# Optimization experiments

Hardware: AMD Instinct MI355X
Metric: run time of the kernel (lower is better)

## Reference

```python
import jax, jax.numpy as jnp
import numpy as np

EPS = 1e-5

def _bn(x, g, b):
    # training-mode BatchNorm1d: batch statistics (biased variance), eps=1e-5
    mean = jnp.mean(x, axis=0)
    var = jnp.mean(jnp.square(x - mean), axis=0)
    return (x - mean) * jax.lax.rsqrt(var + EPS) * g + b

def setup_inputs() -> dict:
    key = jax.random.key(0)
    ks = jax.random.split(key, 16)
    n_nodes, n_edges, d_h, d_e = 50000, 800000, 128, 64
    in_feats, h1, h2, out_feats = 2 * d_h + d_e, 256, 128, 1
    def lin(k, fi, fo):
        bound = 1.0 / np.sqrt(fi)
        kw, kb = jax.random.split(k)
        W = jax.random.uniform(kw, (fo, fi), jnp.float32, -bound, bound)
        b = jax.random.uniform(kb, (fo,), jnp.float32, -bound, bound)
        return W, b
    W1, b1 = lin(ks[0], in_feats, h1)
    W2, b2 = lin(ks[1], h1, h2)
    W3, b3 = lin(ks[2], h2, out_feats)
    return {
        "h": jax.random.normal(ks[3], (n_nodes, d_h), jnp.float32),
        "e": jax.random.normal(ks[4], (n_edges, d_e), jnp.float32),
        "src": jax.random.randint(ks[5], (n_edges,), 0, n_nodes, jnp.int32),
        "dst": jax.random.randint(ks[6], (n_edges,), 0, n_nodes, jnp.int32),
        "bn0_g": jnp.ones((in_feats,), jnp.float32), "bn0_b": jnp.zeros((in_feats,), jnp.float32),
        "W1": W1, "b1": b1,
        "bn1_g": jnp.ones((h1,), jnp.float32), "bn1_b": jnp.zeros((h1,), jnp.float32),
        "W2": W2, "b2": b2,
        "bn2_g": jnp.ones((h2,), jnp.float32), "bn2_b": jnp.zeros((h2,), jnp.float32),
        "W3": W3, "b3": b3,
    }

def reference(h, e, src, dst, bn0_g, bn0_b, W1, b1, bn1_g, bn1_b, W2, b2, bn2_g, bn2_b, W3, b3):
    # edge gather + concat: [n_edges, 2*d_h + d_e]
    x = jnp.concatenate([h[src], h[dst], e], axis=1)
    x = _bn(x, bn0_g, bn0_b)
    x = jnp.maximum(x @ W1.T + b1, 0.0)  # Linear + ReLU (dropout = identity, deterministic)
    x = _bn(x, bn1_g, bn1_b)
    x = jnp.maximum(x @ W2.T + b2, 0.0)
    x = _bn(x, bn2_g, bn2_b)
    return x @ W3.T + b3
```

## Files before the change

kernel.cpp:

```cpp
#include <hip/hip_runtime.h>


#define N_EDGES 800000
#define N_NODES 50000

typedef __attribute__((ext_vector_type(8))) short bf8_t;
typedef __attribute__((ext_vector_type(4))) float f4_t;
typedef __attribute__((ext_vector_type(2))) unsigned int u2_t;
typedef __attribute__((ext_vector_type(4))) unsigned int u4_t;

__device__ __forceinline__ unsigned short f2bf(float f) {
    unsigned int u = __builtin_bit_cast(unsigned int, f);
    u += 0x7FFFu + ((u >> 16) & 1u);
    return (unsigned short)(u >> 16);
}
__device__ __forceinline__ float bf2f(unsigned short s) {
    unsigned int u = ((unsigned int)s) << 16;
    return __builtin_bit_cast(float, u);
}
__device__ __forceinline__ bf8_t cvt8(f4_t x, f4_t y) {
    bf8_t r;
    r[0] = (short)f2bf(x[0]); r[1] = (short)f2bf(x[1]);
    r[2] = (short)f2bf(x[2]); r[3] = (short)f2bf(x[3]);
    r[4] = (short)f2bf(y[0]); r[5] = (short)f2bf(y[1]);
    r[6] = (short)f2bf(y[2]); r[7] = (short)f2bf(y[3]);
    return r;
}

__global__ __launch_bounds__(256) void k_hist(const int* __restrict__ src, const int* __restrict__ dst,
                                              int* __restrict__ cs, int* __restrict__ cd) {
    int i = blockIdx.x * 256 + threadIdx.x;
    if (i < N_EDGES) {
        atomicAdd(&cs[src[i]], 1);
        atomicAdd(&cd[dst[i]], 1);
    }
}

__global__ __launch_bounds__(256) void k_ecvt(const float* __restrict__ e,
        unsigned short* __restrict__ ebf, float* __restrict__ sum, float* __restrict__ sq) {
    const int tid = threadIdx.x;
    const int lane = tid & 63;
    const int cg = tid & 7, rr = tid >> 3;
    f4_t sa = {0.f,0.f,0.f,0.f}, sb = sa, qa = sa, qb = sa;
    for (int r = blockIdx.x * 32 + rr; r < N_EDGES; r += gridDim.x * 32) {
        f4_t va = __builtin_nontemporal_load((const f4_t*)(e + (size_t)r * 64 + cg * 8));
        f4_t vb = __builtin_nontemporal_load((const f4_t*)(e + (size_t)r * 64 + cg * 8 + 4));
        sa += va; qa += va * va; sb += vb; qb += vb * vb;
        bf8_t o = cvt8(va, vb);
        __builtin_nontemporal_store(o,
            (bf8_t*)(ebf + (size_t)(r >> 4) * 1024 + (cg >> 2) * 512 + (((r & 15) << 2) + (cg & 3)) * 8));
    }
#pragma unroll
    for (int d = 8; d <= 32; d <<= 1) {
#pragma unroll
        for (int j = 0; j < 4; ++j) {
            sa[j] += __shfl_xor(sa[j], d); qa[j] += __shfl_xor(qa[j], d);
            sb[j] += __shfl_xor(sb[j], d); qb[j] += __shfl_xor(qb[j], d);
        }
    }
    __shared__ float red[128];
    if (tid < 128) red[tid] = 0.f;
    __syncthreads();
    if (lane < 8) {
#pragma unroll
        for (int j = 0; j < 4; ++j) {
            atomicAdd(&red[lane * 8 + j], sa[j]);
            atomicAdd(&red[lane * 8 + 4 + j], sb[j]);
            atomicAdd(&red[64 + lane * 8 + j], qa[j]);
            atomicAdd(&red[64 + lane * 8 + 4 + j], qb[j]);
        }
    }
    __syncthreads();
    if (tid < 64) atomicAdd(&sum[256 + tid], red[tid]);
    else if (tid < 128) atomicAdd(&sq[256 + tid - 64], red[tid]);
}

__global__ __launch_bounds__(256) void k_hstats(const float* __restrict__ h,
                                                const int* __restrict__ cs, const int* __restrict__ cd,
                                                float* __restrict__ sum, float* __restrict__ sq) {
    const int tid = threadIdx.x;
    const int c = tid & 127, g = tid >> 7;
    float ss = 0.f, qs = 0.f, sd = 0.f, qd = 0.f;
    for (int n = blockIdx.x * 2 + g; n < N_NODES; n += gridDim.x * 2) {
        float v = h[(size_t)n * 128 + c];
        float a = (float)cs[n], b = (float)cd[n];
        ss += a * v; qs += a * v * v;
        sd += b * v; qd += b * v * v;
    }
    __shared__ float red[256];
    red[tid] = ss; __syncthreads();
    if (tid < 128) atomicAdd(&sum[tid], red[tid] + red[tid + 128]);
    __syncthreads();
    red[tid] = qs; __syncthreads();
    if (tid < 128) atomicAdd(&sq[tid], red[tid] + red[tid + 128]);
    __syncthreads();
    red[tid] = sd; __syncthreads();
    if (tid < 128) atomicAdd(&sum[128 + tid], red[tid] + red[tid + 128]);
    __syncthreads();
    red[tid] = qd; __syncthreads();
    if (tid < 128) atomicAdd(&sq[128 + tid], red[tid] + red[tid + 128]);
}

__global__ __launch_bounds__(320) void k_fold0(const float* __restrict__ sum, const float* __restrict__ sq,
        const float* __restrict__ g0, const float* __restrict__ b0,
        float* __restrict__ scale0, float* __restrict__ shift0) {
    int j = threadIdx.x;
    if (j < 320) {
        const float invE = 1.f / (float)N_EDGES;
        float mu = sum[j] * invE;
        float var = sq[j] * invE - mu * mu;
        float sc = g0[j] * rsqrtf(var + 1e-5f);
        scale0[j] = sc;
        shift0[j] = b0[j] - mu * sc;
    }
}

__global__ __launch_bounds__(320) void k_foldW1(const float* __restrict__ W1, const float* __restrict__ b1,
        const float* __restrict__ scale0, const float* __restrict__ shift0,
        unsigned short* __restrict__ W1s, unsigned short* __restrict__ W1d,
        unsigned short* __restrict__ W1e, float* __restrict__ b1p) {
    __shared__ float sc[320], sh[320];
    const int tid = threadIdx.x;
    if (tid < 320) { sc[tid] = scale0[tid]; sh[tid] = shift0[tid]; }
    __syncthreads();
    if (tid < 256) {
        float acc = b1[tid];
        const float* wr = W1 + (size_t)tid * 320;
        for (int j = 0; j < 320; ++j) {
            float wv = wr[j];
            acc += wv * sh[j];
            unsigned short wb = f2bf(wv * sc[j]);
            if (j < 128) W1s[tid * 128 + j] = wb;
            else if (j < 256) W1d[tid * 128 + (j - 128)] = wb;
            else W1e[tid * 64 + (j - 256)] = wb;
        }
        b1p[tid] = acc;
    }
}

__global__ __launch_bounds__(256) void k_P(const float* __restrict__ h,
        const unsigned short* __restrict__ W1s, const unsigned short* __restrict__ W1d,
        unsigned short* __restrict__ Ps, unsigned short* __restrict__ Pd) {
    __shared__ unsigned short tile[16 * 264];
    const int tid = threadIdx.x;
    const int w = tid >> 6, lane = tid & 63, quad = lane >> 4, l15 = lane & 15;
    const unsigned short* W = blockIdx.y ? W1d : W1s;
    unsigned short* P = blockIdx.y ? Pd : Ps;
    const size_t base = (size_t)blockIdx.x * 256;
    bf8_t bfr[4][4];
#pragma unroll
    for (int j = 0; j < 4; ++j) {
        const unsigned short* wp = W + (size_t)((w * 4 + j) * 16 + l15) * 128 + quad * 8;
#pragma unroll
        for (int ks = 0; ks < 4; ++ks) bfr[j][ks] = *(const bf8_t*)(wp + ks * 32);
    }
    const int erow = tid >> 4, ex = tid & 15;
    for (int mc = 0; mc < 16; ++mc) {
        const size_t row0 = base + mc * 16;
        size_t ar = row0 + l15; if (ar >= N_NODES) ar = N_NODES - 1;
        const float* hp = h + ar * 128 + quad * 8;
        bf8_t af[4];
#pragma unroll
        for (int ks = 0; ks < 4; ++ks)
            af[ks] = cvt8(*(const f4_t*)(hp + ks * 32), *(const f4_t*)(hp + ks * 32 + 4));
#pragma unroll
        for (int j = 0; j < 4; ++j) {
            f4_t t = {0.f, 0.f, 0.f, 0.f};
#pragma unroll
            for (int ks = 0; ks < 4; ++ks)
                t = __builtin_amdgcn_mfma_f32_16x16x32_bf16(af[ks], bfr[j][ks], t, 0, 0, 0);
#pragma unroll
            for (int r = 0; r < 4; ++r)
                tile[(quad * 4 + r) * 264 + (w * 4 + j) * 16 + l15] = f2bf(t[r]);
        }
        __syncthreads();
        const size_t orow = row0 + erow;
        if (orow < N_NODES) {
            u4_t v0 = *(const u4_t*)(tile + erow * 264 + ex * 16);
            u4_t v1 = *(const u4_t*)(tile + erow * 264 + ex * 16 + 8);
            *(u4_t*)(P + orow * 256 + ex * 16) = v0;
            *(u4_t*)(P + orow * 256 + ex * 16 + 8) = v1;
        }
        __syncthreads();
    }
}

__global__ __launch_bounds__(256) void k_stats1(const unsigned short* __restrict__ ebf,
        const int* __restrict__ src, const int* __restrict__ dst,
        const unsigned short* __restrict__ Ps, const unsigned short* __restrict__ Pd,
        const unsigned short* __restrict__ W1e, const float* __restrict__ b1p,
        float* __restrict__ slots) {
    __shared__ int sIdx[256], dIdx[256];
    const int tid = threadIdx.x;
    const int w = tid >> 6, lane = tid & 63, quad = lane >> 4, l15 = lane & 15;
    const int perm = l15 * 4 + quad;
    const size_t base = (size_t)blockIdx.x * 256;
    const size_t blk16 = (size_t)blockIdx.x * 16;
    sIdx[tid] = src[base + tid];
    dIdx[tid] = dst[base + tid];
    bf8_t bfr[4][2];
    float bias4[4];
#pragma unroll
    for (int j = 0; j < 4; ++j) {
        const unsigned short* wp = W1e + (size_t)((w * 4 + j) * 16 + l15) * 64 + quad * 8;
        bfr[j][0] = *(const bf8_t*)(wp);
        bfr[j][1] = *(const bf8_t*)(wp + 32);
        bias4[j] = b1p[(w * 4 + j) * 16 + l15];
    }
    const int cb = w * 64 + l15;
    float s[4] = {0.f, 0.f, 0.f, 0.f}, q[4] = {0.f, 0.f, 0.f, 0.f};
    __syncthreads();
    bf8_t af0, af1;
    {
        const unsigned short* ap = ebf + blk16 * 1024 + perm * 8;
        af0 = __builtin_nontemporal_load((const bf8_t*)(ap));
        af1 = __builtin_nontemporal_load((const bf8_t*)(ap + 512));
    }
    for (int mc = 0; mc < 16; ++mc) {
        const int r0 = mc * 16 + quad * 4;
        const unsigned short* p0 = Ps + (size_t)sIdx[r0 + 0] * 256 + cb;
        const unsigned short* p1 = Ps + (size_t)sIdx[r0 + 1] * 256 + cb;
        const unsigned short* p2 = Ps + (size_t)sIdx[r0 + 2] * 256 + cb;
        const unsigned short* p3 = Ps + (size_t)sIdx[r0 + 3] * 256 + cb;
        const unsigned short* d0 = Pd + (size_t)dIdx[r0 + 0] * 256 + cb;
        const unsigned short* d1 = Pd + (size_t)dIdx[r0 + 1] * 256 + cb;
        const unsigned short* d2 = Pd + (size_t)dIdx[r0 + 2] * 256 + cb;
        const unsigned short* d3 = Pd + (size_t)dIdx[r0 + 3] * 256 + cb;
        unsigned short ps[4][4], pd[4][4];
#pragma unroll
        for (int j = 0; j < 4; ++j) {
            ps[0][j] = p0[j * 16]; ps[1][j] = p1[j * 16];
            ps[2][j] = p2[j * 16]; ps[3][j] = p3[j * 16];
            pd[0][j] = d0[j * 16]; pd[1][j] = d1[j * 16];
            pd[2][j] = d2[j * 16]; pd[3][j] = d3[j * 16];
        }
        f4_t acc[4];
#pragma unroll
        for (int j = 0; j < 4; ++j) {
            f4_t t = {0.f, 0.f, 0.f, 0.f};
            t = __builtin_amdgcn_mfma_f32_16x16x32_bf16(af0, bfr[j][0], t, 0, 0, 0);
            acc[j] = __builtin_amdgcn_mfma_f32_16x16x32_bf16(af1, bfr[j][1], t, 0, 0, 0);
        }
        if (mc < 15) {
            const unsigned short* ap = ebf + (blk16 + mc + 1) * 1024 + perm * 8;
            af0 = __builtin_nontemporal_load((const bf8_t*)(ap));
            af1 = __builtin_nontemporal_load((const bf8_t*)(ap + 512));
        }
#pragma unroll
        for (int j = 0; j < 4; ++j)
#pragma unroll
            for (int r = 0; r < 4; ++r) {
                float v = acc[j][r] + bf2f(ps[r][j]) + bf2f(pd[r][j]) + bias4[j];
                v = fmaxf(v, 0.f);
                s[j] += v; q[j] += v * v;
            }
    }
#pragma unroll
    for (int j = 0; j < 4; ++j) {
        s[j] += __shfl_xor(s[j], 16); s[j] += __shfl_xor(s[j], 32);
        q[j] += __shfl_xor(q[j], 16); q[j] += __shfl_xor(q[j], 32);
    }
    if (lane < 16) {
        float* sl = slots + (size_t)(blockIdx.x & 63) * 512;
#pragma unroll
        for (int j = 0; j < 4; ++j) {
            atomicAdd(&sl[cb + j * 16], s[j]);
            atomicAdd(&sl[256 + cb + j * 16], q[j]);
        }
    }
}

__global__ __launch_bounds__(256) void k_fold1(const float* __restrict__ slots,
        const float* __restrict__ g1, const float* __restrict__ b1n,
        const float* __restrict__ W2, const float* __restrict__ b2,
        unsigned short* __restrict__ W2p, float* __restrict__ b2p) {
    __shared__ float sc[256], sh[256];
    const int tid = threadIdx.x;
    float S = 0.f, Q = 0.f;
    for (int s = 0; s < 64; ++s) { S += slots[s * 512 + tid]; Q += slots[s * 512 + 256 + tid]; }
    const float invE = 1.f / (float)N_EDGES;
    float mu = S * invE;
    float var = Q * invE - mu * mu;
    float scl = g1[tid] * rsqrtf(var + 1e-5f);
    sc[tid] = scl; sh[tid] = b1n[tid] - mu * scl;
    __syncthreads();
    if (tid < 128) {
        float acc = b2[tid];
        const float* wr = W2 + (size_t)tid * 256;
        for (int j = 0; j < 256; ++j) {
            float wv = wr[j];
            acc += wv * sh[j];
            W2p[tid * 256 + j] = f2bf(wv * sc[j]);
        }
        b2p[tid] = acc;
    }
}

__global__ __launch_bounds__(256) void k_L12(const unsigned short* __restrict__ ebf,
        const int* __restrict__ src, const int* __restrict__ dst,
        const unsigned short* __restrict__ Ps, const unsigned short* __restrict__ Pd,
        const unsigned short* __restrict__ W1e, const float* __restrict__ b1p,
        const unsigned short* __restrict__ W2p, const float* __restrict__ b2p,
        unsigned short* __restrict__ a2c, float* __restrict__ slots) {
    __shared__ unsigned short tile1[16 * 264];
    __shared__ unsigned short tile2[2][4096];
    __shared__ int sIdx[256], dIdx[256];
    const int tid = threadIdx.x;
    const int w = tid >> 6, lane = tid & 63, quad = lane >> 4, l15 = lane & 15;
    const int perm = l15 * 4 + quad;
    const size_t base = (size_t)blockIdx.x * 256;
    const size_t blk16 = (size_t)blockIdx.x * 16;
    sIdx[tid] = src[base + tid];
    dIdx[tid] = dst[base + tid];
    bf8_t bfr1[4][2];
    float bias4[4];
#pragma unroll
    for (int j = 0; j < 4; ++j) {
        const unsigned short* wp = W1e + (size_t)((w * 4 + j) * 16 + l15) * 64 + quad * 8;
        bfr1[j][0] = *(const bf8_t*)(wp);
        bfr1[j][1] = *(const bf8_t*)(wp + 32);
        bias4[j] = b1p[(w * 4 + j) * 16 + l15];
    }
    bf8_t bfr2[2][8];
    float bias2[2];
#pragma unroll
    for (int j = 0; j < 2; ++j) {
        const unsigned short* wp = W2p + (size_t)((w * 2 + j) * 16 + l15) * 256 + quad * 8;
#pragma unroll
        for (int ks = 0; ks < 8; ++ks) bfr2[j][ks] = *(const bf8_t*)(wp + ks * 32);
        bias2[j] = b2p[(w * 2 + j) * 16 + l15];
    }
    const int erow = tid >> 4, ex = tid & 15;
    float s0 = 0.f, q0 = 0.f, s1 = 0.f, q1 = 0.f;
    __syncthreads();
    bf8_t af0, af1;
    u4_t gs0, gs1, gd0, gd1;
    {
        const unsigned short* ap = ebf + blk16 * 1024 + perm * 8;
        af0 = __builtin_nontemporal_load((const bf8_t*)(ap));
        af1 = __builtin_nontemporal_load((const bf8_t*)(ap + 512));
        const size_t sr = (size_t)sIdx[erow] * 256, dr = (size_t)dIdx[erow] * 256;
        gs0 = *(const u4_t*)(Ps + sr + ex * 8);
        gs1 = *(const u4_t*)(Ps + sr + ex * 8 + 128);
        gd0 = *(const u4_t*)(Pd + dr + ex * 8);
        gd1 = *(const u4_t*)(Pd + dr + ex * 8 + 128);
    }
    for (int mc = 0; mc < 16; ++mc) {
        unsigned short* t2 = tile2[mc & 1];
#pragma unroll
        for (int j = 0; j < 4; ++j) {
            f4_t t = {0.f, 0.f, 0.f, 0.f};
            t = __builtin_amdgcn_mfma_f32_16x16x32_bf16(af0, bfr1[j][0], t, 0, 0, 0);
            t = __builtin_amdgcn_mfma_f32_16x16x32_bf16(af1, bfr1[j][1], t, 0, 0, 0);
#pragma unroll
            for (int r = 0; r < 4; ++r)
                tile1[(quad * 4 + r) * 264 + (w * 4 + j) * 16 + l15] = f2bf(t[r] + bias4[j]);
        }
        if (mc < 15) {
            const unsigned short* ap = ebf + (blk16 + mc + 1) * 1024 + perm * 8;
            af0 = __builtin_nontemporal_load((const bf8_t*)(ap));
            af1 = __builtin_nontemporal_load((const bf8_t*)(ap + 512));
        }
        __syncthreads();
#pragma unroll
        for (int i = 0; i < 2; ++i) {
            u4_t tv = *(const u4_t*)(&tile1[erow * 264 + ex * 8 + 128 * i]);
            const unsigned short* tu = (const unsigned short*)&tv;
            const unsigned short* su = (const unsigned short*)(i ? &gs1 : &gs0);
            const unsigned short* du = (const unsigned short*)(i ? &gd1 : &gd0);
            unsigned short ov[8];
#pragma unroll
            for (int j = 0; j < 8; ++j) {
                float v = bf2f(tu[j]) + bf2f(su[j]) + bf2f(du[j]);
                ov[j] = f2bf(fmaxf(v, 0.f));
            }
            *(u4_t*)(&t2[((ex >> 2) + 4 * i) * 512 + (erow * 4 + (ex & 3)) * 8]) = *(const u4_t*)ov;
        }
        if (mc < 15) {
            const size_t sr = (size_t)sIdx[(mc + 1) * 16 + erow] * 256;
            const size_t dr = (size_t)dIdx[(mc + 1) * 16 + erow] * 256;
            gs0 = *(const u4_t*)(Ps + sr + ex * 8);
            gs1 = *(const u4_t*)(Ps + sr + ex * 8 + 128);
            gd0 = *(const u4_t*)(Pd + dr + ex * 8);
            gd1 = *(const u4_t*)(Pd + dr + ex * 8 + 128);
        }
        __syncthreads();
        f4_t acc0 = {0.f, 0.f, 0.f, 0.f}, acc1 = acc0;
#pragma unroll
        for (int ks = 0; ks < 8; ++ks) {
            bf8_t a = *(const bf8_t*)(&t2[ks * 512 + perm * 8]);
            acc0 = __builtin_amdgcn_mfma_f32_16x16x32_bf16(a, bfr2[0][ks], acc0, 0, 0, 0);
            acc1 = __builtin_amdgcn_mfma_f32_16x16x32_bf16(a, bfr2[1][ks], acc1, 0, 0, 0);
        }
        unsigned short* outp = a2c + (blk16 + mc) * 2048;
        unsigned short pv[4];
#pragma unroll
        for (int r = 0; r < 4; ++r) {
            float v = fmaxf(acc0[r] + bias2[0], 0.f);
            pv[r] = f2bf(v); s0 += v; q0 += v * v;
        }
        __builtin_nontemporal_store(*(const u2_t*)pv,
            (u2_t*)(outp + (((w * 2) * 16 + l15) * 4 + quad) * 4));
#pragma unroll
        for (int r = 0; r < 4; ++r) {
            float v = fmaxf(acc1[r] + bias2[1], 0.f);
            pv[r] = f2bf(v); s1 += v; q1 += v * v;
        }
        __builtin_nontemporal_store(*(const u2_t*)pv,
            (u2_t*)(outp + (((w * 2 + 1) * 16 + l15) * 4 + quad) * 4));
    }
    s0 += __shfl_xor(s0, 16); s0 += __shfl_xor(s0, 32);
    q0 += __shfl_xor(q0, 16); q0 += __shfl_xor(q0, 32);
    s1 += __shfl_xor(s1, 16); s1 += __shfl_xor(s1, 32);
    q1 += __shfl_xor(q1, 16); q1 += __shfl_xor(q1, 32);
    if (lane < 16) {
        float* sl = slots + (size_t)(blockIdx.x & 63) * 256;
        const int c0 = (w * 2) * 16 + l15;
        atomicAdd(&sl[c0], s0); atomicAdd(&sl[128 + c0], q0);
        atomicAdd(&sl[c0 + 16], s1); atomicAdd(&sl[128 + c0 + 16], q1);
    }
}

__global__ __launch_bounds__(128) void k_fold2(const float* __restrict__ slots,
        const float* __restrict__ g2, const float* __restrict__ b2n,
        const float* __restrict__ W3, const float* __restrict__ b3,
        float* __restrict__ w3p, float* __restrict__ b3p) {
    __shared__ float red[128];
    const int tid = threadIdx.x;
    float S = 0.f, Q = 0.f;
    for (int s = 0; s < 64; ++s) { S += slots[s * 256 + tid]; Q += slots[s * 256 + 128 + tid]; }
    const float invE = 1.f / (float)N_EDGES;
    float mu = S * invE;
    float var = Q * invE - mu * mu;
    float scl = g2[tid] * rsqrtf(var + 1e-5f);
    float shf = b2n[tid] - mu * scl;
    w3p[tid] = W3[tid] * scl;
    red[tid] = W3[tid] * shf;
    __syncthreads();
    for (int st = 64; st > 0; st >>= 1) {
        if (tid < st) red[tid] += red[tid + st];
        __syncthreads();
    }
    if (tid == 0) b3p[0] = b3[0] + red[0];
}

__global__ __launch_bounds__(256) void k_L3(const unsigned short* __restrict__ a2c,
        const float* __restrict__ w3p, const float* __restrict__ b3p, float* __restrict__ out) {
    __shared__ float wl[128];
    const int tid = threadIdx.x;
    if (tid < 128) wl[tid] = w3p[tid];
    __syncthreads();
    const int w = tid >> 6, lane = tid & 63, q = lane >> 4, c = lane & 15;
    const float bb = b3p[0];
#pragma unroll
    for (int i = 0; i < 4; ++i) {
        const size_t b = (size_t)blockIdx.x * 16 + w * 4 + i;
        const unsigned short* bp = a2c + b * 2048 + c * 16 + q * 4;
        float a0 = 0.f, a1r = 0.f, a2r = 0.f, a3r = 0.f;
#pragma unroll
        for (int jt = 0; jt < 8; ++jt) {
            u2_t v = __builtin_nontemporal_load((const u2_t*)(bp + jt * 256));
            const unsigned short* u = (const unsigned short*)&v;
            const float wv = wl[jt * 16 + c];
            a0 += bf2f(u[0]) * wv; a1r += bf2f(u[1]) * wv;
            a2r += bf2f(u[2]) * wv; a3r += bf2f(u[3]) * wv;
        }
#pragma unroll
        for (int d = 1; d <= 8; d <<= 1) {
            a0 += __shfl_xor(a0, d); a1r += __shfl_xor(a1r, d);
            a2r += __shfl_xor(a2r, d); a3r += __shfl_xor(a3r, d);
        }
        if (c == 0) {
            f4_t o = {a0 + bb, a1r + bb, a2r + bb, a3r + bb};
            *(f4_t*)(out + b * 16 + q * 4) = o;
        }
    }
}

extern "C" void kernel_launch(void* const* d_in, const int* in_sizes, int n_in,
                              void* d_out, int out_size, void* d_ws, size_t ws_size,
                              hipStream_t stream) {
    (void)in_sizes; (void)n_in; (void)out_size; (void)ws_size;
    const float* h   = (const float*)d_in[0];
    const float* e   = (const float*)d_in[1];
    const int*   src = (const int*)d_in[2];
    const int*   dst = (const int*)d_in[3];
    const float* bn0_g = (const float*)d_in[4];
    const float* bn0_b = (const float*)d_in[5];
    const float* W1 = (const float*)d_in[6];
    const float* b1 = (const float*)d_in[7];
    const float* bn1_g = (const float*)d_in[8];
    const float* bn1_b = (const float*)d_in[9];
    const float* W2 = (const float*)d_in[10];
    const float* b2 = (const float*)d_in[11];
    const float* bn2_g = (const float*)d_in[12];
    const float* bn2_b = (const float*)d_in[13];
    const float* W3 = (const float*)d_in[14];
    const float* b3 = (const float*)d_in[15];

    char* ws = (char*)d_ws;
    size_t off = 0;
    auto alloc = [&](size_t bytes) { char* p = ws + off; off += (bytes + 255) & ~(size_t)255; return p; };
    int*   cnt_s = (int*)alloc((size_t)N_NODES * 4);
    int*   cnt_d = (int*)alloc((size_t)N_NODES * 4);
    float* bn0_sum = (float*)alloc(320 * 4);
    float* bn0_sq  = (float*)alloc(320 * 4);
    float* bn1_slots = (float*)alloc(64 * 512 * 4);
    float* bn2_slots = (float*)alloc(64 * 256 * 4);
    const size_t zero_end = off;
    float* scale0 = (float*)alloc(320 * 4);
    float* shift0 = (float*)alloc(320 * 4);
    unsigned short* W1s = (unsigned short*)alloc(256 * 128 * 2);
    unsigned short* W1d = (unsigned short*)alloc(256 * 128 * 2);
    unsigned short* W1e = (unsigned short*)alloc(256 * 64 * 2);
    float* b1p = (float*)alloc(256 * 4);
    unsigned short* W2p = (unsigned short*)alloc(128 * 256 * 2);
    float* b2p = (float*)alloc(128 * 4);
    float* w3p = (float*)alloc(128 * 4);
    float* b3p = (float*)alloc(4);
    unsigned short* Ps = (unsigned short*)alloc((size_t)N_NODES * 256 * 2);
    unsigned short* Pd = (unsigned short*)alloc((size_t)N_NODES * 256 * 2);
    unsigned short* ebf = (unsigned short*)alloc((size_t)(N_EDGES / 16) * 2048);
    unsigned short* a2c = (unsigned short*)alloc((size_t)(N_EDGES / 16) * 4096);

    hipMemsetAsync(d_ws, 0, zero_end, stream);
    k_hist<<<(N_EDGES + 255) / 256, 256, 0, stream>>>(src, dst, cnt_s, cnt_d);
    k_ecvt<<<512, 256, 0, stream>>>(e, ebf, bn0_sum, bn0_sq);
    k_hstats<<<200, 256, 0, stream>>>(h, cnt_s, cnt_d, bn0_sum, bn0_sq);
    k_fold0<<<1, 320, 0, stream>>>(bn0_sum, bn0_sq, bn0_g, bn0_b, scale0, shift0);
    k_foldW1<<<1, 320, 0, stream>>>(W1, b1, scale0, shift0, W1s, W1d, W1e, b1p);
    k_P<<<dim3(196, 2), 256, 0, stream>>>(h, W1s, W1d, Ps, Pd);
    k_stats1<<<N_EDGES / 256, 256, 0, stream>>>(ebf, src, dst, Ps, Pd, W1e, b1p, bn1_slots);
    k_fold1<<<1, 256, 0, stream>>>(bn1_slots, bn1_g, bn1_b, W2, b2, W2p, b2p);
    k_L12<<<N_EDGES / 256, 256, 0, stream>>>(ebf, src, dst, Ps, Pd, W1e, b1p, W2p, b2p, a2c, bn2_slots);
    k_fold2<<<1, 128, 0, stream>>>(bn2_slots, bn2_g, bn2_b, W3, b3, w3p, b3p);
    k_L3<<<N_EDGES / 256, 256, 0, stream>>>(a2c, w3p, b3p, (float*)d_out);
}
```

Baseline: 1.050 ms.

## Sort edges by destination and remap blocks per XCD for gather locality

Adds a counting sort of edges by destination node (scan plus atomic scatter) and processes edges in sorted order, with the edge features permuted during bf16 conversion and outputs scattered back through the permutation. Block IDs in the two main kernels are remapped so that consecutive edge chunks land on the same XCD, improving L2 reuse of the gathered Ps/Pd rows. It also folds biases into the MFMA accumulator init, keeps the layer-1 tile in fp32 in LDS, and sets occupancy launch bounds on k_L12. The cost is extra sort kernels, a serial single-block scan, gathered reads of e, and scattered output writes.

Result: slower. 1.762 ms (+67.9%).

```diff
diff --git a/kernel.cpp b/kernel.cpp
--- a/kernel.cpp
+++ b/kernel.cpp
@@ -36,19 +36,56 @@
     }
 }
 
-__global__ __launch_bounds__(256) void k_ecvt(const float* __restrict__ e,
+__global__ __launch_bounds__(256) void k_scan(const int* __restrict__ bh, int* __restrict__ boff) {
+    __shared__ int part[256];
+    __shared__ int excl[256];
+    const int t = threadIdx.x;
+    const int base = t * 196;
+    int s = 0;
+    for (int j = 0; j < 196; ++j) {
+        int idx = base + j;
+        if (idx < N_NODES) s += bh[idx];
+    }
+    part[t] = s;
+    __syncthreads();
+    if (t == 0) {
+        int r = 0;
+        for (int i = 0; i < 256; ++i) { excl[i] = r; r += part[i]; }
+    }
+    __syncthreads();
+    int r = excl[t];
+    for (int j = 0; j < 196; ++j) {
+        int idx = base + j;
+        if (idx < N_NODES) { boff[idx] = r; r += bh[idx]; }
+    }
+}
+
+__global__ __launch_bounds__(256) void k_scatter(const int* __restrict__ src, const int* __restrict__ dst,
+        int* __restrict__ boff, int* __restrict__ sSrc, int* __restrict__ sDst, int* __restrict__ perm) {
+    int i = blockIdx.x * 256 + threadIdx.x;
+    if (i < N_EDGES) {
+        int d = dst[i];
+        int pos = atomicAdd(&boff[d], 1);
+        sSrc[pos] = src[i];
+        sDst[pos] = d;
+        perm[pos] = i;
+    }
+}
+
+__global__ __launch_bounds__(256) void k_ecvt(const float* __restrict__ e, const int* __restrict__ perm,
         unsigned short* __restrict__ ebf, float* __restrict__ sum, float* __restrict__ sq) {
     const int tid = threadIdx.x;
     const int lane = tid & 63;
     const int cg = tid & 7, rr = tid >> 3;
     f4_t sa = {0.f,0.f,0.f,0.f}, sb = sa, qa = sa, qb = sa;
-    for (int r = blockIdx.x * 32 + rr; r < N_EDGES; r += gridDim.x * 32) {
-        f4_t va = __builtin_nontemporal_load((const f4_t*)(e + (size_t)r * 64 + cg * 8));
-        f4_t vb = __builtin_nontemporal_load((const f4_t*)(e + (size_t)r * 64 + cg * 8 + 4));
+    for (int p = blockIdx.x * 32 + rr; p < N_EDGES; p += gridDim.x * 32) {
+        const int row = perm[p];
+        f4_t va = __builtin_nontemporal_load((const f4_t*)(e + (size_t)row * 64 + cg * 8));
+        f4_t vb = __builtin_nontemporal_load((const f4_t*)(e + (size_t)row * 64 + cg * 8 + 4));
         sa += va; qa += va * va; sb += vb; qb += vb * vb;
         bf8_t o = cvt8(va, vb);
         __builtin_nontemporal_store(o,
-            (bf8_t*)(ebf + (size_t)(r >> 4) * 1024 + (cg >> 2) * 512 + (((r & 15) << 2) + (cg & 3)) * 8));
+            (bf8_t*)(ebf + (size_t)(p >> 4) * 1024 + (cg >> 2) * 512 + (((p & 15) << 2) + (cg & 3)) * 8));
     }
 #pragma unroll
     for (int d = 8; d <= 32; d <<= 1) {
@@ -194,8 +231,12 @@
     const int tid = threadIdx.x;
     const int w = tid >> 6, lane = tid & 63, quad = lane >> 4, l15 = lane & 15;
     const int perm = l15 * 4 + quad;
-    const size_t base = (size_t)blockIdx.x * 256;
-    const size_t blk16 = (size_t)blockIdx.x * 16;
+    const int nwg = gridDim.x;
+    const int qq = nwg >> 3, r8 = nwg & 7;
+    const int xcd = blockIdx.x & 7, seq = blockIdx.x >> 3;
+    const int bid = (xcd < r8 ? xcd * (qq + 1) : r8 * (qq + 1) + (xcd - r8) * qq) + seq;
+    const size_t base = (size_t)bid * 256;
+    const size_t blk16 = (size_t)bid * 16;
     sIdx[tid] = src[base + tid];
     dIdx[tid] = dst[base + tid];
     bf8_t bfr[4][2];
@@ -237,7 +278,7 @@
         f4_t acc[4];
 #pragma unroll
         for (int j = 0; j < 4; ++j) {
-            f4_t t = {0.f, 0.f, 0.f, 0.f};
+            f4_t t = {bias4[j], bias4[j], bias4[j], bias4[j]};
             t = __builtin_amdgcn_mfma_f32_16x16x32_bf16(af0, bfr[j][0], t, 0, 0, 0);
             acc[j] = __builtin_amdgcn_mfma_f32_16x16x32_bf16(af1, bfr[j][1], t, 0, 0, 0);
         }
@@ -250,7 +291,7 @@
         for (int j = 0; j < 4; ++j)
 #pragma unroll
             for (int r = 0; r < 4; ++r) {
-                float v = acc[j][r] + bf2f(ps[r][j]) + bf2f(pd[r][j]) + bias4[j];
+                float v = acc[j][r] + bf2f(ps[r][j]) + bf2f(pd[r][j]);
                 v = fmaxf(v, 0.f);
                 s[j] += v; q[j] += v * v;
             }
@@ -261,7 +302,7 @@
         q[j] += __shfl_xor(q[j], 16); q[j] += __shfl_xor(q[j], 32);
     }
     if (lane < 16) {
-        float* sl = slots + (size_t)(blockIdx.x & 63) * 512;
+        float* sl = slots + (size_t)(bid & 63) * 512;
 #pragma unroll
         for (int j = 0; j < 4; ++j) {
             atomicAdd(&sl[cb + j * 16], s[j]);
@@ -296,20 +337,24 @@
     }
 }
 
-__global__ __launch_bounds__(256) void k_L12(const unsigned short* __restrict__ ebf,
+__global__ __launch_bounds__(256, 4) void k_L12(const unsigned short* __restrict__ ebf,
         const int* __restrict__ src, const int* __restrict__ dst,
         const unsigned short* __restrict__ Ps, const unsigned short* __restrict__ Pd,
         const unsigned short* __restrict__ W1e, const float* __restrict__ b1p,
         const unsigned short* __restrict__ W2p, const float* __restrict__ b2p,
         unsigned short* __restrict__ a2c, float* __restrict__ slots) {
-    __shared__ unsigned short tile1[16 * 264];
+    __shared__ __align__(16) float tile1[16 * 268];
     __shared__ unsigned short tile2[2][4096];
     __shared__ int sIdx[256], dIdx[256];
     const int tid = threadIdx.x;
     const int w = tid >> 6, lane = tid & 63, quad = lane >> 4, l15 = lane & 15;
     const int perm = l15 * 4 + quad;
-    const size_t base = (size_t)blockIdx.x * 256;
-    const size_t blk16 = (size_t)blockIdx.x * 16;
+    const int nwg = gridDim.x;
+    const int qq = nwg >> 3, r8 = nwg & 7;
+    const int xcd = blockIdx.x & 7, seq = blockIdx.x >> 3;
+    const int bid = (xcd < r8 ? xcd * (qq + 1) : r8 * (qq + 1) + (xcd - r8) * qq) + seq;
+    const size_t base = (size_t)bid * 256;
+    const size_t blk16 = (size_t)bid * 16;
     sIdx[tid] = src[base + tid];
     dIdx[tid] = dst[base + tid];
     bf8_t bfr1[4][2];
@@ -349,12 +394,12 @@
         unsigned short* t2 = tile2[mc & 1];
 #pragma unroll
         for (int j = 0; j < 4; ++j) {
-            f4_t t = {0.f, 0.f, 0.f, 0.f};
+            f4_t t = {bias4[j], bias4[j], bias4[j], bias4[j]};
             t = __builtin_amdgcn_mfma_f32_16x16x32_bf16(af0, bfr1[j][0], t, 0, 0, 0);
             t = __builtin_amdgcn_mfma_f32_16x16x32_bf16(af1, bfr1[j][1], t, 0, 0, 0);
 #pragma unroll
             for (int r = 0; r < 4; ++r)
-                tile1[(quad * 4 + r) * 264 + (w * 4 + j) * 16 + l15] = f2bf(t[r] + bias4[j]);
+                tile1[(quad * 4 + r) * 268 + (w * 4 + j) * 16 + l15] = t[r];
         }
         if (mc < 15) {
             const unsigned short* ap = ebf + (blk16 + mc + 1) * 1024 + perm * 8;
@@ -364,15 +409,21 @@
         __syncthreads();
 #pragma unroll
         for (int i = 0; i < 2; ++i) {
-            u4_t tv = *(const u4_t*)(&tile1[erow * 264 + ex * 8 + 128 * i]);
-            const unsigned short* tu = (const unsigned short*)&tv;
+            const float* tp = tile1 + erow * 268 + ex * 8 + 128 * i;
+            f4_t tv0 = *(const f4_t*)tp;
+            f4_t tv1 = *(const f4_t*)(tp + 4);
             const unsigned short* su = (const unsigned short*)(i ? &gs1 : &gs0);
             const unsigned short* du = (const unsigned short*)(i ? &gd1 : &gd0);
             unsigned short ov[8];
 #pragma unroll
-            for (int j = 0; j < 8; ++j) {
-                float v = bf2f(tu[j]) + bf2f(su[j]) + bf2f(du[j]);
+            for (int j = 0; j < 4; ++j) {
+                float v = tv0[j] + bf2f(su[j]) + bf2f(du[j]);
                 ov[j] = f2bf(fmaxf(v, 0.f));
+            }
+#pragma unroll
+            for (int j = 0; j < 4; ++j) {
+                float v = tv1[j] + bf2f(su[4 + j]) + bf2f(du[4 + j]);
+                ov[4 + j] = f2bf(fmaxf(v, 0.f));
             }
             *(u4_t*)(&t2[((ex >> 2) + 4 * i) * 512 + (erow * 4 + (ex & 3)) * 8]) = *(const u4_t*)ov;
         }
@@ -385,7 +436,8 @@
             gd1 = *(const u4_t*)(Pd + dr + ex * 8 + 128);
         }
         __syncthreads();
-        f4_t acc0 = {0.f, 0.f, 0.f, 0.f}, acc1 = acc0;
+        f4_t acc0 = {bias2[0], bias2[0], bias2[0], bias2[0]};
+        f4_t acc1 = {bias2[1], bias2[1], bias2[1], bias2[1]};
 #pragma unroll
         for (int ks = 0; ks < 8; ++ks) {
             bf8_t a = *(const bf8_t*)(&t2[ks * 512 + perm * 8]);
@@ -396,14 +448,14 @@
         unsigned short pv[4];
 #pragma unroll
         for (int r = 0; r < 4; ++r) {
-            float v = fmaxf(acc0[r] + bias2[0], 0.f);
+            float v = fmaxf(acc0[r], 0.f);
             pv[r] = f2bf(v); s0 += v; q0 += v * v;
         }
         __builtin_nontemporal_store(*(const u2_t*)pv,
             (u2_t*)(outp + (((w * 2) * 16 + l15) * 4 + quad) * 4));
 #pragma unroll
         for (int r = 0; r < 4; ++r) {
-            float v = fmaxf(acc1[r] + bias2[1], 0.f);
+            float v = fmaxf(acc1[r], 0.f);
             pv[r] = f2bf(v); s1 += v; q1 += v * v;
         }
         __builtin_nontemporal_store(*(const u2_t*)pv,
@@ -414,7 +466,7 @@
     s1 += __shfl_xor(s1, 16); s1 += __shfl_xor(s1, 32);
     q1 += __shfl_xor(q1, 16); q1 += __shfl_xor(q1, 32);
     if (lane < 16) {
-        float* sl = slots + (size_t)(blockIdx.x & 63) * 256;
+        float* sl = slots + (size_t)(bid & 63) * 256;
         const int c0 = (w * 2) * 16 + l15;
         atomicAdd(&sl[c0], s0); atomicAdd(&sl[128 + c0], q0);
         atomicAdd(&sl[c0 + 16], s1); atomicAdd(&sl[128 + c0 + 16], q1);
@@ -445,6 +497,7 @@
 }
 
 __global__ __launch_bounds__(256) void k_L3(const unsigned short* __restrict__ a2c,
+        const int* __restrict__ perm,
         const float* __restrict__ w3p, const float* __restrict__ b3p, float* __restrict__ out) {
     __shared__ float wl[128];
     const int tid = threadIdx.x;
@@ -471,8 +524,11 @@
             a2r += __shfl_xor(a2r, d); a3r += __shfl_xor(a3r, d);
         }
         if (c == 0) {
-            f4_t o = {a0 + bb, a1r + bb, a2r + bb, a3r + bb};
-            *(f4_t*)(out + b * 16 + q * 4) = o;
+            const int4 pi = *(const int4*)(perm + b * 16 + q * 4);
+            out[pi.x] = a0 + bb;
+            out[pi.y] = a1r + bb;
+            out[pi.z] = a2r + bb;
+            out[pi.w] = a3r + bb;
         }
     }
 }
@@ -508,6 +564,10 @@
     float* bn1_slots = (float*)alloc(64 * 512 * 4);
     float* bn2_slots = (float*)alloc(64 * 256 * 4);
     const size_t zero_end = off;
+    int*   boff = (int*)alloc((size_t)N_NODES * 4);
+    int*   sSrc = (int*)alloc((size_t)N_EDGES * 4);
+    int*   sDst = (int*)alloc((size_t)N_EDGES * 4);
+    int*   perm = (int*)alloc((size_t)N_EDGES * 4);
     float* scale0 = (float*)alloc(320 * 4);
     float* shift0 = (float*)alloc(320 * 4);
     unsigned short* W1s = (unsigned short*)alloc(256 * 128 * 2);
@@ -525,14 +585,16 @@
 
     hipMemsetAsync(d_ws, 0, zero_end, stream);
     k_hist<<<(N_EDGES + 255) / 256, 256, 0, stream>>>(src, dst, cnt_s, cnt_d);
-    k_ecvt<<<512, 256, 0, stream>>>(e, ebf, bn0_sum, bn0_sq);
+    k_scan<<<1, 256, 0, stream>>>(cnt_d, boff);
+    k_scatter<<<(N_EDGES + 255) / 256, 256, 0, stream>>>(src, dst, boff, sSrc, sDst, perm);
+    k_ecvt<<<512, 256, 0, stream>>>(e, perm, ebf, bn0_sum, bn0_sq);
     k_hstats<<<200, 256, 0, stream>>>(h, cnt_s, cnt_d, bn0_sum, bn0_sq);
     k_fold0<<<1, 320, 0, stream>>>(bn0_sum, bn0_sq, bn0_g, bn0_b, scale0, shift0);
     k_foldW1<<<1, 320, 0, stream>>>(W1, b1, scale0, shift0, W1s, W1d, W1e, b1p);
     k_P<<<dim3(196, 2), 256, 0, stream>>>(h, W1s, W1d, Ps, Pd);
-    k_stats1<<<N_EDGES / 256, 256, 0, stream>>>(ebf, src, dst, Ps, Pd, W1e, b1p, bn1_slots);
+    k_stats1<<<N_EDGES / 256, 256, 0, stream>>>(ebf, sSrc, sDst, Ps, Pd, W1e, b1p, bn1_slots);
     k_fold1<<<1, 256, 0, stream>>>(bn1_slots, bn1_g, bn1_b, W2, b2, W2p, b2p);
-    k_L12<<<N_EDGES / 256, 256, 0, stream>>>(ebf, src, dst, Ps, Pd, W1e, b1p, W2p, b2p, a2c, bn2_slots);
+    k_L12<<<N_EDGES / 256, 256, 0, stream>>>(ebf, sSrc, sDst, Ps, Pd, W1e, b1p, W2p, b2p, a2c, bn2_slots);
     k_fold2<<<1, 128, 0, stream>>>(bn2_slots, bn2_g, bn2_b, W3, b3, w3p, b3p);
-    k_L3<<<N_EDGES / 256, 256, 0, stream>>>(a2c, w3p, b3p, (float*)d_out);
-}
+    k_L3<<<N_EDGES / 256, 256, 0, stream>>>(a2c, perm, w3p, b3p, (float*)d_out);
+}
```
